# Optimization experiments

Hardware: AMD Instinct MI355X
Metric: run time of the kernel (lower is better)

Reference implementation:

```python
import jax, jax.numpy as jnp
import numpy as np

B, HORIZON, F, ORDER, K = 8192, 64, 64, 16, 256


def setup_inputs() -> dict:
    key = jax.random.key(0)
    ks = jax.random.split(key, 7)
    s = 0.05
    x = jax.random.normal(ks[0], (B, HORIZON, F), dtype=jnp.float32)
    y0 = jax.random.normal(ks[1], (B, ORDER), dtype=jnp.float32)
    kernel = jax.random.normal(ks[2], (F + ORDER, 4 * K), dtype=jnp.float32) * s
    rec_kernel = jax.random.normal(ks[3], (K, 4 * K), dtype=jnp.float32) * s
    bias = jax.random.normal(ks[4], (4 * K,), dtype=jnp.float32) * s
    dense_w = jax.random.normal(ks[5], (K, 1), dtype=jnp.float32) * s
    dense_b = jax.random.normal(ks[6], (1,), dtype=jnp.float32) * s
    return {"x": x, "y0": y0, "kernel": kernel, "rec_kernel": rec_kernel,
            "bias": bias, "dense_w": dense_w, "dense_b": dense_b}


def reference(x, y0, kernel, rec_kernel, bias, dense_w, dense_b):
    Bn = x.shape[0]
    Ku = rec_kernel.shape[0]
    h0 = jnp.zeros((Bn, Ku), x.dtype)
    c0 = jnp.zeros((Bn, Ku), x.dtype)

    def step(carry, x_t):
        h, c, yp = carry  # yp: [B, order], newest prediction first
        inp = jnp.concatenate([x_t, yp], axis=1)          # [B, F+order]
        z = inp @ kernel + h @ rec_kernel + bias          # [B, 4K]
        i, f, g, o = jnp.split(z, 4, axis=1)              # Keras gate order i,f,c,o
        i = jax.nn.sigmoid(i)
        f = jax.nn.sigmoid(f)
        g = jnp.tanh(g)
        o = jax.nn.sigmoid(o)
        c_new = f * c + i * g
        h_new = o * jnp.tanh(c_new)
        pred = h_new @ dense_w + dense_b                  # [B, 1]
        # tf.roll(shift=1)[:, 1:] then concat([pred, .]) == shift-in newest pred
        yp_new = jnp.concatenate([pred, yp[:, :-1]], axis=1)
        return (h_new, c_new, yp_new), pred

    xs = jnp.transpose(x, (1, 0, 2))                      # [horizon, B, F]
    _, preds = jax.lax.scan(step, (h0, c0, y0), xs)       # preds: [horizon, B, 1]
    return jnp.transpose(preds, (1, 0, 2))                # [B, horizon, 1]
```

## Files before the change

### kernel.cpp

```cpp
#include <hip/hip_runtime.h>
#include <stdint.h>


typedef short v8s __attribute__((ext_vector_type(8)));
typedef float v4f __attribute__((ext_vector_type(4)));

#define NKS 11
#define NKCOL 1024
#define PKR 1
#define PKL 2
#define SK0 (PKR + PKL)

__device__ __forceinline__ unsigned bf16u(float f) {
  unsigned u = __float_as_uint(f);
  return (u + 0x7FFFu + ((u >> 16) & 1u)) >> 16;
}
__device__ __forceinline__ float sigm(float x) {
  return __builtin_amdgcn_rcpf(1.f + __expf(-x));
}
__device__ __forceinline__ float tanh_(float x) {
  return 1.f - 2.f * __builtin_amdgcn_rcpf(1.f + __expf(2.f * x));
}
__device__ __forceinline__ int a_addr(int m, int k) {
  return (((m >> 4) * NKS + (k >> 5)) << 10)
       + ((((k >> 3) & 3) * 16 + (m & 15)) << 4)
       + ((k & 7) << 1);
}

__global__ void prep_w(const float* __restrict__ ker, const float* __restrict__ rec,
                       uint4* __restrict__ wsw) {
  int tid = blockIdx.x * 256 + threadIdx.x;
  int lane = tid & 63;
  int rest = tid >> 6;
  int ks = rest % NKS;
  int nt = rest / NKS;
  int n  = nt * 16 + (lane & 15);
  int k0 = ks * 32 + ((lane >> 4) & 3) * 8;
  unsigned h[8];
  #pragma unroll
  for (int j = 0; j < 8; ++j) {
    int k = k0 + j;
    float v = 0.f;
    if (k < 80)       v = ker[k * NKCOL + n];
    else if (k < 336) v = rec[(k - 80) * NKCOL + n];
    h[j] = bf16u(v);
  }
  uint4 o;
  o.x = h[0] | (h[1] << 16); o.y = h[2] | (h[3] << 16);
  o.z = h[4] | (h[5] << 16); o.w = h[6] | (h[7] << 16);
  wsw[tid] = o;
}

__global__ __launch_bounds__(512, 2)
void lstm_main(const float* __restrict__ x, const float* __restrict__ y0,
               const float* __restrict__ bias, const float* __restrict__ dw,
               const float* __restrict__ db, const v8s* __restrict__ wv,
               float* __restrict__ out) {
  __shared__ __align__(16) char a_lds[2 * NKS * 1024];
  __shared__ __align__(16) v8s w_lds[PKL * 64 * 64];
  __shared__ float predbuf[32][8];
  __shared__ float predf[32];

  const int tid  = threadIdx.x;
  const int lane = tid & 63;
  const int wave = tid >> 6;
  const int l15  = lane & 15;
  const int quad = lane >> 4;
  const int b0   = blockIdx.x * 32;

  for (int i = tid; i < 2 * NKS * 256; i += 512) ((unsigned*)a_lds)[i] = 0;
  for (int i = tid; i < PKL * 64 * 64; i += 512) {
    int ksl = i >> 12;
    int nt  = (i >> 6) & 63;
    int ln  = i & 63;
    w_lds[i] = wv[(nt * NKS + PKR + ksl) * 64 + ln];
  }

  float bias_v[8];
  int wb[8], wlo[8];
  #pragma unroll
  for (int ln = 0; ln < 8; ++ln) {
    int g = ln >> 1, s = ln & 1;
    int ntg = g * 16 + wave * 2 + s;
    wb[ln]  = ntg * NKS * 64;
    wlo[ln] = ntg * 64 + lane;
    bias_v[ln] = bias[ntg * 16 + l15];
  }
  float dw_v[2];
  dw_v[0] = dw[wave * 32 + l15];
  dw_v[1] = dw[wave * 32 + 16 + l15];
  const float dbv = db[0];

  v8s wreg[8];
  #pragma unroll
  for (int ln = 0; ln < 8; ++ln)
    wreg[ln] = wv[wb[ln] + lane];

  float cst[2][2][4];
  #pragma unroll
  for (int mt = 0; mt < 2; ++mt)
    #pragma unroll
    for (int s = 0; s < 2; ++s)
      #pragma unroll
      for (int r = 0; r < 4; ++r) cst[mt][s][r] = 0.f;

  const int ms_x  = tid >> 3;
  const int kq8_x = tid & 7;
  const int ms_y  = (tid - 256) >> 3;
  const int jj    = tid & 7;
  float4 xpa, xpb;
  if (tid < 256) {
    const float* xp = x + ((size_t)((b0 + ms_x) * 64)) * 64 + kq8_x * 8;
    xpa = ((const float4*)xp)[0];
    xpb = ((const float4*)xp)[1];
  }

  __syncthreads();

  #pragma unroll 1
  for (int t = 0; t < 64; ++t) {
    unsigned xw[4];
    unsigned short q0 = 0, q1 = 0;
    float pin = 0.f;
    if (tid < 256) {
      xw[0] = bf16u(xpa.x) | (bf16u(xpa.y) << 16);
      xw[1] = bf16u(xpa.z) | (bf16u(xpa.w) << 16);
      xw[2] = bf16u(xpb.x) | (bf16u(xpb.y) << 16);
      xw[3] = bf16u(xpb.z) | (bf16u(xpb.w) << 16);
    } else {
      if (t == 0) {
        q0 = (unsigned short)bf16u(y0[(b0 + ms_y) * 16 + 2 * jj]);
        q1 = (unsigned short)bf16u(y0[(b0 + ms_y) * 16 + 2 * jj + 1]);
      } else {
        q0 = *(const unsigned short*)(a_lds + a_addr(ms_y, 64 + 2 * jj));
        q1 = *(const unsigned short*)(a_lds + a_addr(ms_y, 64 + 2 * jj + 1));
        pin = predf[ms_y];
      }
    }
    __syncthreads();
    if (tid < 256) {
      uint4 w4; w4.x = xw[0]; w4.y = xw[1]; w4.z = xw[2]; w4.w = xw[3];
      *(uint4*)(a_lds + a_addr(ms_x, kq8_x * 8)) = w4;
    } else {
      if (t == 0) {
        *(unsigned short*)(a_lds + a_addr(ms_y, 64 + 2 * jj))     = q0;
        *(unsigned short*)(a_lds + a_addr(ms_y, 64 + 2 * jj + 1)) = q1;
      } else {
        if (jj < 7) {
          *(unsigned short*)(a_lds + a_addr(ms_y, 64 + 2 * jj + 1)) = q0;
          *(unsigned short*)(a_lds + a_addr(ms_y, 64 + 2 * jj + 2)) = q1;
        } else {
          *(unsigned short*)(a_lds + a_addr(ms_y, 79)) = q0;
        }
        if (jj == 0)
          *(unsigned short*)(a_lds + a_addr(ms_y, 64)) = (unsigned short)bf16u(pin);
      }
    }
    __syncthreads();

    if (t < 63 && tid < 256) {
      const float* xp = x + ((size_t)((b0 + ms_x) * 64 + (t + 1))) * 64 + kq8_x * 8;
      xpa = ((const float4*)xp)[0];
      xpb = ((const float4*)xp)[1];
    }

    v4f acc[2][8];
    #pragma unroll
    for (int mt = 0; mt < 2; ++mt)
      #pragma unroll
      for (int ln = 0; ln < 8; ++ln) acc[mt][ln] = v4f{0.f, 0.f, 0.f, 0.f};

    v8s bs0[8], bs1[8];
    #pragma unroll
    for (int ln = 0; ln < 8; ++ln) bs0[ln] = wv[wb[ln] + SK0 * 64 + lane];
    v8s af0 = *(const v8s*)(a_lds + (lane << 4));
    v8s af1 = *(const v8s*)(a_lds + (NKS << 10) + (lane << 4));

    #define MFMA_BLK(ksi, W8)                                                   \
      do {                                                                      \
        v8s c0 = af0, c1 = af1;                                                 \
        if ((ksi) < NKS - 1) {                                                  \
          af0 = *(const v8s*)(a_lds + (((ksi) + 1) << 10) + (lane << 4));       \
          af1 = *(const v8s*)(a_lds + ((NKS + (ksi) + 1) << 10) + (lane << 4)); \
        }                                                                       \
        _Pragma("unroll")                                                       \
        for (int ln = 0; ln < 8; ++ln) {                                        \
          acc[0][ln] = __builtin_amdgcn_mfma_f32_16x16x32_bf16(c0, W8[ln], acc[0][ln], 0, 0, 0); \
          acc[1][ln] = __builtin_amdgcn_mfma_f32_16x16x32_bf16(c1, W8[ln], acc[1][ln], 0, 0, 0); \
        }                                                                       \
      } while (0)
    #define REFILL(BUF, rks)                                                    \
      do {                                                                      \
        _Pragma("unroll")                                                       \
        for (int ln = 0; ln < 8; ++ln)                                          \
          BUF[ln] = wv[wb[ln] + (rks) * 64 + lane];                             \
      } while (0)

    MFMA_BLK(0, wreg);

    {
      v8s wl[8];
      #pragma unroll
      for (int ln = 0; ln < 8; ++ln) wl[ln] = w_lds[wlo[ln]];
      REFILL(bs1, SK0 + 1);
      MFMA_BLK(1, wl);
      #pragma unroll
      for (int ln = 0; ln < 8; ++ln) wl[ln] = w_lds[4096 + wlo[ln]];
      MFMA_BLK(2, wl);
    }

    MFMA_BLK(3, bs0);  REFILL(bs0, 5);
    MFMA_BLK(4, bs1);  REFILL(bs1, 6);
    MFMA_BLK(5, bs0);  REFILL(bs0, 7);
    MFMA_BLK(6, bs1);  REFILL(bs1, 8);
    MFMA_BLK(7, bs0);  REFILL(bs0, 9);
    MFMA_BLK(8, bs1);  REFILL(bs1, 10);
    MFMA_BLK(9, bs0);
    MFMA_BLK(10, bs1);

    #undef MFMA_BLK
    #undef REFILL

    __syncthreads();

    float padd[2][4];
    #pragma unroll
    for (int mt = 0; mt < 2; ++mt)
      #pragma unroll
      for (int r = 0; r < 4; ++r) padd[mt][r] = 0.f;

    #pragma unroll
    for (int mt = 0; mt < 2; ++mt) {
      #pragma unroll
      for (int s = 0; s < 2; ++s) {
        const int kk = 80 + wave * 32 + s * 16 + l15;
        #pragma unroll
        for (int r = 0; r < 4; ++r) {
          float zi = acc[mt][0 + s][r] + bias_v[0 + s];
          float zf = acc[mt][2 + s][r] + bias_v[2 + s];
          float zg = acc[mt][4 + s][r] + bias_v[4 + s];
          float zo = acc[mt][6 + s][r] + bias_v[6 + s];
          float is = sigm(zi), fs = sigm(zf), gs = tanh_(zg), os = sigm(zo);
          float cn = fs * cst[mt][s][r] + is * gs;
          cst[mt][s][r] = cn;
          float hh = os * tanh_(cn);
          int m = mt * 16 + quad * 4 + r;
          *(unsigned short*)(a_lds + a_addr(m, kk)) = (unsigned short)bf16u(hh);
          padd[mt][r] += hh * dw_v[s];
        }
      }
    }
    #pragma unroll
    for (int mt = 0; mt < 2; ++mt) {
      #pragma unroll
      for (int r = 0; r < 4; ++r) {
        float p = padd[mt][r];
        p += __shfl_xor(p, 1);
        p += __shfl_xor(p, 2);
        p += __shfl_xor(p, 4);
        p += __shfl_xor(p, 8);
        if (l15 == 0) predbuf[mt * 16 + quad * 4 + r][wave] = p;
      }
    }
    __syncthreads();
    if (tid < 32) {
      float p = dbv;
      #pragma unroll
      for (int w = 0; w < 8; ++w) p += predbuf[tid][w];
      out[(size_t)(b0 + tid) * 64 + t] = p;
      predf[tid] = p;
    }
    __syncthreads();
  }
}

extern "C" void kernel_launch(void* const* d_in, const int* in_sizes, int n_in,
                              void* d_out, int out_size, void* d_ws, size_t ws_size,
                              hipStream_t stream) {
  const float* x    = (const float*)d_in[0];
  const float* y0   = (const float*)d_in[1];
  const float* ker  = (const float*)d_in[2];
  const float* rec  = (const float*)d_in[3];
  const float* bias = (const float*)d_in[4];
  const float* dw   = (const float*)d_in[5];
  const float* db   = (const float*)d_in[6];

  prep_w<<<dim3(176), dim3(256), 0, stream>>>(ker, rec, (uint4*)d_ws);
  lstm_main<<<dim3(256), dim3(512), 0, stream>>>(x, y0, bias, dw, db,
                                                 (const v8s*)d_ws, (float*)d_out);
}
```

Measured before the change: 1.292 ms.

## Pin second weight k-slice in registers, prefetch across steps, and drop a barrier

```diff
diff --git a/kernel.cpp b/kernel.cpp
--- a/kernel.cpp
+++ b/kernel.cpp
@@ -7,7 +7,7 @@
 
 #define NKS 11
 #define NKCOL 1024
-#define PKR 1
+#define PKR 2
 #define PKL 2
 #define SK0 (PKR + PKL)
 
@@ -20,6 +20,12 @@
 }
 __device__ __forceinline__ float tanh_(float x) {
   return 1.f - 2.f * __builtin_amdgcn_rcpf(1.f + __expf(2.f * x));
+}
+__device__ __forceinline__ void bar_lds() {
+  __builtin_amdgcn_sched_barrier(0);
+  asm volatile("s_waitcnt lgkmcnt(0)" ::: "memory");
+  __builtin_amdgcn_s_barrier();
+  __builtin_amdgcn_sched_barrier(0);
 }
 __device__ __forceinline__ int a_addr(int m, int k) {
   return (((m >> 4) * NKS + (k >> 5)) << 10)
@@ -91,10 +97,12 @@
   dw_v[1] = dw[wave * 32 + 16 + l15];
   const float dbv = db[0];
 
-  v8s wreg[8];
-  #pragma unroll
-  for (int ln = 0; ln < 8; ++ln)
-    wreg[ln] = wv[wb[ln] + lane];
+  v8s wreg0[8], wreg1[8];
+  #pragma unroll
+  for (int ln = 0; ln < 8; ++ln) {
+    wreg0[ln] = wv[wb[ln] + lane];
+    wreg1[ln] = wv[wb[ln] + 64 + lane];
+  }
 
   float cst[2][2][4];
   #pragma unroll
@@ -103,6 +111,17 @@
     for (int s = 0; s < 2; ++s)
       #pragma unroll
       for (int r = 0; r < 4; ++r) cst[mt][s][r] = 0.f;
+
+  #define REFILL(BUF, rks)                                                    \
+    do {                                                                      \
+      _Pragma("unroll")                                                       \
+      for (int ln = 0; ln < 8; ++ln)                                          \
+        BUF[ln] = wv[wb[ln] + (rks) * 64 + lane];                             \
+    } while (0)
+
+  v8s bs0[8], bs1[8];
+  REFILL(bs0, SK0);
+  REFILL(bs1, SK0 + 1);
 
   const int ms_x  = tid >> 3;
   const int kq8_x = tid & 7;
@@ -119,33 +138,24 @@
 
   #pragma unroll 1
   for (int t = 0; t < 64; ++t) {
-    unsigned xw[4];
-    unsigned short q0 = 0, q1 = 0;
-    float pin = 0.f;
     if (tid < 256) {
-      xw[0] = bf16u(xpa.x) | (bf16u(xpa.y) << 16);
-      xw[1] = bf16u(xpa.z) | (bf16u(xpa.w) << 16);
-      xw[2] = bf16u(xpb.x) | (bf16u(xpb.y) << 16);
-      xw[3] = bf16u(xpb.z) | (bf16u(xpb.w) << 16);
-    } else {
-      if (t == 0) {
-        q0 = (unsigned short)bf16u(y0[(b0 + ms_y) * 16 + 2 * jj]);
-        q1 = (unsigned short)bf16u(y0[(b0 + ms_y) * 16 + 2 * jj + 1]);
-      } else {
-        q0 = *(const unsigned short*)(a_lds + a_addr(ms_y, 64 + 2 * jj));
-        q1 = *(const unsigned short*)(a_lds + a_addr(ms_y, 64 + 2 * jj + 1));
-        pin = predf[ms_y];
-      }
-    }
-    __syncthreads();
-    if (tid < 256) {
-      uint4 w4; w4.x = xw[0]; w4.y = xw[1]; w4.z = xw[2]; w4.w = xw[3];
+      uint4 w4;
+      w4.x = bf16u(xpa.x) | (bf16u(xpa.y) << 16);
+      w4.y = bf16u(xpa.z) | (bf16u(xpa.w) << 16);
+      w4.z = bf16u(xpb.x) | (bf16u(xpb.y) << 16);
+      w4.w = bf16u(xpb.z) | (bf16u(xpb.w) << 16);
       *(uint4*)(a_lds + a_addr(ms_x, kq8_x * 8)) = w4;
     } else {
       if (t == 0) {
+        unsigned short q0 = (unsigned short)bf16u(y0[(b0 + ms_y) * 16 + 2 * jj]);
+        unsigned short q1 = (unsigned short)bf16u(y0[(b0 + ms_y) * 16 + 2 * jj + 1]);
         *(unsigned short*)(a_lds + a_addr(ms_y, 64 + 2 * jj))     = q0;
         *(unsigned short*)(a_lds + a_addr(ms_y, 64 + 2 * jj + 1)) = q1;
       } else {
+        unsigned short q0 = *(const unsigned short*)(a_lds + a_addr(ms_y, 64 + 2 * jj));
+        unsigned short q1 = *(const unsigned short*)(a_lds + a_addr(ms_y, 64 + 2 * jj + 1));
+        float pin = predf[ms_y];
+        __builtin_amdgcn_sched_barrier(0);
         if (jj < 7) {
           *(unsigned short*)(a_lds + a_addr(ms_y, 64 + 2 * jj + 1)) = q0;
           *(unsigned short*)(a_lds + a_addr(ms_y, 64 + 2 * jj + 2)) = q1;
@@ -156,7 +166,7 @@
           *(unsigned short*)(a_lds + a_addr(ms_y, 64)) = (unsigned short)bf16u(pin);
       }
     }
-    __syncthreads();
+    bar_lds();
 
     if (t < 63 && tid < 256) {
       const float* xp = x + ((size_t)((b0 + ms_x) * 64 + (t + 1))) * 64 + kq8_x * 8;
@@ -170,9 +180,11 @@
       #pragma unroll
       for (int ln = 0; ln < 8; ++ln) acc[mt][ln] = v4f{0.f, 0.f, 0.f, 0.f};
 
-    v8s bs0[8], bs1[8];
-    #pragma unroll
-    for (int ln = 0; ln < 8; ++ln) bs0[ln] = wv[wb[ln] + SK0 * 64 + lane];
+    v8s wla[8], wlb[8];
+    #pragma unroll
+    for (int ln = 0; ln < 8; ++ln) wla[ln] = w_lds[wlo[ln]];
+    #pragma unroll
+    for (int ln = 0; ln < 8; ++ln) wlb[ln] = w_lds[4096 + wlo[ln]];
     v8s af0 = *(const v8s*)(a_lds + (lane << 4));
     v8s af1 = *(const v8s*)(a_lds + (NKS << 10) + (lane << 4));
 
@@ -189,39 +201,22 @@
           acc[1][ln] = __builtin_amdgcn_mfma_f32_16x16x32_bf16(c1, W8[ln], acc[1][ln], 0, 0, 0); \
         }                                                                       \
       } while (0)
-    #define REFILL(BUF, rks)                                                    \
-      do {                                                                      \
-        _Pragma("unroll")                                                       \
-        for (int ln = 0; ln < 8; ++ln)                                          \
-          BUF[ln] = wv[wb[ln] + (rks) * 64 + lane];                             \
-      } while (0)
-
-    MFMA_BLK(0, wreg);
-
-    {
-      v8s wl[8];
-      #pragma unroll
-      for (int ln = 0; ln < 8; ++ln) wl[ln] = w_lds[wlo[ln]];
-      REFILL(bs1, SK0 + 1);
-      MFMA_BLK(1, wl);
-      #pragma unroll
-      for (int ln = 0; ln < 8; ++ln) wl[ln] = w_lds[4096 + wlo[ln]];
-      MFMA_BLK(2, wl);
-    }
-
-    MFMA_BLK(3, bs0);  REFILL(bs0, 5);
-    MFMA_BLK(4, bs1);  REFILL(bs1, 6);
-    MFMA_BLK(5, bs0);  REFILL(bs0, 7);
-    MFMA_BLK(6, bs1);  REFILL(bs1, 8);
-    MFMA_BLK(7, bs0);  REFILL(bs0, 9);
-    MFMA_BLK(8, bs1);  REFILL(bs1, 10);
-    MFMA_BLK(9, bs0);
-    MFMA_BLK(10, bs1);
+
+    MFMA_BLK(0, wreg0);
+    MFMA_BLK(1, wreg1);
+    MFMA_BLK(2, wla);
+    MFMA_BLK(3, wlb);
+    MFMA_BLK(4, bs0);   REFILL(bs0, 6);
+    MFMA_BLK(5, bs1);   REFILL(bs1, 7);
+    MFMA_BLK(6, bs0);   REFILL(bs0, 8);
+    MFMA_BLK(7, bs1);   REFILL(bs1, 9);
+    MFMA_BLK(8, bs0);   REFILL(bs0, 10);
+    MFMA_BLK(9, bs1);   REFILL(bs1, SK0 + 1);
+    MFMA_BLK(10, bs0);  REFILL(bs0, SK0);
 
     #undef MFMA_BLK
-    #undef REFILL
-
-    __syncthreads();
+
+    bar_lds();
 
     float padd[2][4];
     #pragma unroll
@@ -262,7 +257,7 @@
         if (l15 == 0) predbuf[mt * 16 + quad * 4 + r][wave] = p;
       }
     }
-    __syncthreads();
+    bar_lds();
     if (tid < 32) {
       float p = dbv;
       #pragma unroll
@@ -270,8 +265,9 @@
       out[(size_t)(b0 + tid) * 64 + t] = p;
       predf[tid] = p;
     }
-    __syncthreads();
-  }
+    bar_lds();
+  }
+  #undef REFILL
 }
 
 extern "C" void kernel_launch(void* const* d_in, const int* in_sizes, int n_in,
```

Measured after the change: 2.136 ms. 65.4% more time.

## Split LSTM gate columns across 16 waves per block instead of 8

Applied to the files above, without the earlier changes.

```diff
diff --git a/kernel.cpp b/kernel.cpp
--- a/kernel.cpp
+++ b/kernel.cpp
@@ -7,9 +7,8 @@
 
 #define NKS 11
 #define NKCOL 1024
-#define PKR 1
 #define PKL 2
-#define SK0 (PKR + PKL)
+#define SK0 PKL
 
 __device__ __forceinline__ unsigned bf16u(float f) {
   unsigned u = __float_as_uint(f);
@@ -51,14 +50,14 @@
   wsw[tid] = o;
 }
 
-__global__ __launch_bounds__(512, 2)
+__global__ __launch_bounds__(1024, 4)
 void lstm_main(const float* __restrict__ x, const float* __restrict__ y0,
                const float* __restrict__ bias, const float* __restrict__ dw,
                const float* __restrict__ db, const v8s* __restrict__ wv,
                float* __restrict__ out) {
   __shared__ __align__(16) char a_lds[2 * NKS * 1024];
   __shared__ __align__(16) v8s w_lds[PKL * 64 * 64];
-  __shared__ float predbuf[32][8];
+  __shared__ float predbuf[32][16];
   __shared__ float predf[32];
 
   const int tid  = threadIdx.x;
@@ -68,41 +67,42 @@
   const int quad = lane >> 4;
   const int b0   = blockIdx.x * 32;
 
-  for (int i = tid; i < 2 * NKS * 256; i += 512) ((unsigned*)a_lds)[i] = 0;
-  for (int i = tid; i < PKL * 64 * 64; i += 512) {
+  for (int i = tid; i < 2 * NKS * 256; i += 1024) ((unsigned*)a_lds)[i] = 0;
+  for (int i = tid; i < PKL * 64 * 64; i += 1024) {
     int ksl = i >> 12;
     int nt  = (i >> 6) & 63;
     int ln  = i & 63;
-    w_lds[i] = wv[(nt * NKS + PKR + ksl) * 64 + ln];
-  }
-
-  float bias_v[8];
-  int wb[8], wlo[8];
+    w_lds[i] = wv[(nt * NKS + ksl) * 64 + ln];
+  }
+
+  float bias_v[4];
+  int wb[4], wlo[4];
   #pragma unroll
-  for (int ln = 0; ln < 8; ++ln) {
-    int g = ln >> 1, s = ln & 1;
-    int ntg = g * 16 + wave * 2 + s;
-    wb[ln]  = ntg * NKS * 64;
-    wlo[ln] = ntg * 64 + lane;
-    bias_v[ln] = bias[ntg * 16 + l15];
-  }
-  float dw_v[2];
-  dw_v[0] = dw[wave * 32 + l15];
-  dw_v[1] = dw[wave * 32 + 16 + l15];
-  const float dbv = db[0];
-
-  v8s wreg[8];
-  #pragma unroll
-  for (int ln = 0; ln < 8; ++ln)
-    wreg[ln] = wv[wb[ln] + lane];
-
-  float cst[2][2][4];
+  for (int g = 0; g < 4; ++g) {
+    int ntg = g * 16 + wave;
+    wb[g]  = ntg * NKS * 64;
+    wlo[g] = ntg * 64 + lane;
+    bias_v[g] = bias[ntg * 16 + l15];
+  }
+  const float dw_v = dw[wave * 16 + l15];
+  const float dbv  = db[0];
+
+  float cst[2][4];
   #pragma unroll
   for (int mt = 0; mt < 2; ++mt)
     #pragma unroll
-    for (int s = 0; s < 2; ++s)
-      #pragma unroll
-      for (int r = 0; r < 4; ++r) cst[mt][s][r] = 0.f;
+    for (int r = 0; r < 4; ++r) cst[mt][r] = 0.f;
+
+  #define REFILL(BUF, rks)                                                    \
+    do {                                                                      \
+      _Pragma("unroll")                                                       \
+      for (int g = 0; g < 4; ++g)                                             \
+        BUF[g] = wv[wb[g] + (rks) * 64 + lane];                               \
+    } while (0)
+
+  v8s bs0[4], bs1[4];
+  REFILL(bs0, SK0);
+  REFILL(bs1, SK0 + 1);
 
   const int ms_x  = tid >> 3;
   const int kq8_x = tid & 7;
@@ -127,7 +127,7 @@
       xw[1] = bf16u(xpa.z) | (bf16u(xpa.w) << 16);
       xw[2] = bf16u(xpb.x) | (bf16u(xpb.y) << 16);
       xw[3] = bf16u(xpb.z) | (bf16u(xpb.w) << 16);
-    } else {
+    } else if (tid < 512) {
       if (t == 0) {
         q0 = (unsigned short)bf16u(y0[(b0 + ms_y) * 16 + 2 * jj]);
         q1 = (unsigned short)bf16u(y0[(b0 + ms_y) * 16 + 2 * jj + 1]);
@@ -141,7 +141,7 @@
     if (tid < 256) {
       uint4 w4; w4.x = xw[0]; w4.y = xw[1]; w4.z = xw[2]; w4.w = xw[3];
       *(uint4*)(a_lds + a_addr(ms_x, kq8_x * 8)) = w4;
-    } else {
+    } else if (tid < 512) {
       if (t == 0) {
         *(unsigned short*)(a_lds + a_addr(ms_y, 64 + 2 * jj))     = q0;
         *(unsigned short*)(a_lds + a_addr(ms_y, 64 + 2 * jj + 1)) = q1;
@@ -158,25 +158,16 @@
     }
     __syncthreads();
 
-    if (t < 63 && tid < 256) {
-      const float* xp = x + ((size_t)((b0 + ms_x) * 64 + (t + 1))) * 64 + kq8_x * 8;
-      xpa = ((const float4*)xp)[0];
-      xpb = ((const float4*)xp)[1];
-    }
-
-    v4f acc[2][8];
+    v4f acc[2][4];
     #pragma unroll
     for (int mt = 0; mt < 2; ++mt)
       #pragma unroll
-      for (int ln = 0; ln < 8; ++ln) acc[mt][ln] = v4f{0.f, 0.f, 0.f, 0.f};
-
-    v8s bs0[8], bs1[8];
-    #pragma unroll
-    for (int ln = 0; ln < 8; ++ln) bs0[ln] = wv[wb[ln] + SK0 * 64 + lane];
+      for (int g = 0; g < 4; ++g) acc[mt][g] = v4f{0.f, 0.f, 0.f, 0.f};
+
     v8s af0 = *(const v8s*)(a_lds + (lane << 4));
     v8s af1 = *(const v8s*)(a_lds + (NKS << 10) + (lane << 4));
 
-    #define MFMA_BLK(ksi, W8)                                                   \
+    #define MFMA_BLK(ksi, W4)                                                   \
       do {                                                                      \
         v8s c0 = af0, c1 = af1;                                                 \
         if ((ksi) < NKS - 1) {                                                  \
@@ -184,70 +175,59 @@
           af1 = *(const v8s*)(a_lds + ((NKS + (ksi) + 1) << 10) + (lane << 4)); \
         }                                                                       \
         _Pragma("unroll")                                                       \
-        for (int ln = 0; ln < 8; ++ln) {                                        \
-          acc[0][ln] = __builtin_amdgcn_mfma_f32_16x16x32_bf16(c0, W8[ln], acc[0][ln], 0, 0, 0); \
-          acc[1][ln] = __builtin_amdgcn_mfma_f32_16x16x32_bf16(c1, W8[ln], acc[1][ln], 0, 0, 0); \
+        for (int g = 0; g < 4; ++g) {                                           \
+          acc[0][g] = __builtin_amdgcn_mfma_f32_16x16x32_bf16(c0, W4[g], acc[0][g], 0, 0, 0); \
+          acc[1][g] = __builtin_amdgcn_mfma_f32_16x16x32_bf16(c1, W4[g], acc[1][g], 0, 0, 0); \
         }                                                                       \
       } while (0)
-    #define REFILL(BUF, rks)                                                    \
-      do {                                                                      \
-        _Pragma("unroll")                                                       \
-        for (int ln = 0; ln < 8; ++ln)                                          \
-          BUF[ln] = wv[wb[ln] + (rks) * 64 + lane];                             \
-      } while (0)
-
-    MFMA_BLK(0, wreg);
 
     {
-      v8s wl[8];
-      #pragma unroll
-      for (int ln = 0; ln < 8; ++ln) wl[ln] = w_lds[wlo[ln]];
-      REFILL(bs1, SK0 + 1);
-      MFMA_BLK(1, wl);
-      #pragma unroll
-      for (int ln = 0; ln < 8; ++ln) wl[ln] = w_lds[4096 + wlo[ln]];
-      MFMA_BLK(2, wl);
-    }
-
-    MFMA_BLK(3, bs0);  REFILL(bs0, 5);
-    MFMA_BLK(4, bs1);  REFILL(bs1, 6);
-    MFMA_BLK(5, bs0);  REFILL(bs0, 7);
-    MFMA_BLK(6, bs1);  REFILL(bs1, 8);
-    MFMA_BLK(7, bs0);  REFILL(bs0, 9);
-    MFMA_BLK(8, bs1);  REFILL(bs1, 10);
-    MFMA_BLK(9, bs0);
-    MFMA_BLK(10, bs1);
+      v8s wl0[4];
+      #pragma unroll
+      for (int g = 0; g < 4; ++g) wl0[g] = w_lds[wlo[g]];
+      MFMA_BLK(0, wl0);
+      v8s wl1[4];
+      #pragma unroll
+      for (int g = 0; g < 4; ++g) wl1[g] = w_lds[4096 + wlo[g]];
+      MFMA_BLK(1, wl1);
+    }
+    MFMA_BLK(2, bs0);   REFILL(bs0, 4);
+    MFMA_BLK(3, bs1);   REFILL(bs1, 5);
+    MFMA_BLK(4, bs0);   REFILL(bs0, 6);
+    MFMA_BLK(5, bs1);   REFILL(bs1, 7);
+    MFMA_BLK(6, bs0);   REFILL(bs0, 8);
+    MFMA_BLK(7, bs1);   REFILL(bs1, 9);
+    MFMA_BLK(8, bs0);   REFILL(bs0, 10);
+    MFMA_BLK(9, bs1);   REFILL(bs1, SK0 + 1);
+    MFMA_BLK(10, bs0);  REFILL(bs0, SK0);
 
     #undef MFMA_BLK
-    #undef REFILL
-
-    __syncthreads();
-
+
+    __syncthreads();
+
+    if (t < 63 && tid < 256) {
+      const float* xp = x + ((size_t)((b0 + ms_x) * 64 + (t + 1))) * 64 + kq8_x * 8;
+      xpa = ((const float4*)xp)[0];
+      xpb = ((const float4*)xp)[1];
+    }
+
+    const int kk = 80 + wave * 16 + l15;
     float padd[2][4];
     #pragma unroll
-    for (int mt = 0; mt < 2; ++mt)
-      #pragma unroll
-      for (int r = 0; r < 4; ++r) padd[mt][r] = 0.f;
-
-    #pragma unroll
     for (int mt = 0; mt < 2; ++mt) {
       #pragma unroll
-      for (int s = 0; s < 2; ++s) {
-        const int kk = 80 + wave * 32 + s * 16 + l15;
-        #pragma unroll
-        for (int r = 0; r < 4; ++r) {
-          float zi = acc[mt][0 + s][r] + bias_v[0 + s];
-          float zf = acc[mt][2 + s][r] + bias_v[2 + s];
-          float zg = acc[mt][4 + s][r] + bias_v[4 + s];
-          float zo = acc[mt][6 + s][r] + bias_v[6 + s];
-          float is = sigm(zi), fs = sigm(zf), gs = tanh_(zg), os = sigm(zo);
-          float cn = fs * cst[mt][s][r] + is * gs;
-          cst[mt][s][r] = cn;
-          float hh = os * tanh_(cn);
-          int m = mt * 16 + quad * 4 + r;
-          *(unsigned short*)(a_lds + a_addr(m, kk)) = (unsigned short)bf16u(hh);
-          padd[mt][r] += hh * dw_v[s];
-        }
+      for (int r = 0; r < 4; ++r) {
+        float zi = acc[mt][0][r] + bias_v[0];
+        float zf = acc[mt][1][r] + bias_v[1];
+        float zg = acc[mt][2][r] + bias_v[2];
+        float zo = acc[mt][3][r] + bias_v[3];
+        float is = sigm(zi), fs = sigm(zf), gs = tanh_(zg), os = sigm(zo);
+        float cn = fs * cst[mt][r] + is * gs;
+        cst[mt][r] = cn;
+        float hh = os * tanh_(cn);
+        int m = mt * 16 + quad * 4 + r;
+        *(unsigned short*)(a_lds + a_addr(m, kk)) = (unsigned short)bf16u(hh);
+        padd[mt][r] = hh * dw_v;
       }
     }
     #pragma unroll
@@ -266,12 +246,13 @@
     if (tid < 32) {
       float p = dbv;
       #pragma unroll
-      for (int w = 0; w < 8; ++w) p += predbuf[tid][w];
+      for (int w = 0; w < 16; ++w) p += predbuf[tid][w];
       out[(size_t)(b0 + tid) * 64 + t] = p;
       predf[tid] = p;
     }
     __syncthreads();
   }
+  #undef REFILL
 }
 
 extern "C" void kernel_launch(void* const* d_in, const int* in_sizes, int n_in,
@@ -286,6 +267,6 @@
   const float* db   = (const float*)d_in[6];
 
   prep_w<<<dim3(176), dim3(256), 0, stream>>>(ker, rec, (uint4*)d_ws);
-  lstm_main<<<dim3(256), dim3(512), 0, stream>>>(x, y0, bias, dw, db,
-                                                 (const v8s*)d_ws, (float*)d_out);
-}
+  lstm_main<<<dim3(256), dim3(1024), 0, stream>>>(x, y0, bias, dw, db,
+                                                  (const v8s*)d_ws, (float*)d_out);
+}
```

Result: slower. 1.578 ms (+22.1%).

## Double batch rows per block to reuse streamed weights across four M-tiles

Applied to the files above, without the earlier changes.

```diff
diff --git a/kernel.cpp b/kernel.cpp
--- a/kernel.cpp
+++ b/kernel.cpp
@@ -7,9 +7,7 @@
 
 #define NKS 11
 #define NKCOL 1024
-#define PKR 1
-#define PKL 2
-#define SK0 (PKR + PKL)
+#define MT 4
 
 __device__ __forceinline__ unsigned bf16u(float f) {
   unsigned u = __float_as_uint(f);
@@ -56,24 +54,22 @@
                const float* __restrict__ bias, const float* __restrict__ dw,
                const float* __restrict__ db, const v8s* __restrict__ wv,
                float* __restrict__ out) {
-  __shared__ __align__(16) char a_lds[2 * NKS * 1024];
-  __shared__ __align__(16) v8s w_lds[PKL * 64 * 64];
-  __shared__ float predbuf[32][8];
-  __shared__ float predf[32];
+  __shared__ __align__(16) char a_lds[MT * NKS * 1024];
+  __shared__ __align__(16) v8s w_lds[64 * 64];
+  __shared__ float predbuf[64][8];
+  __shared__ float predf[64];
 
   const int tid  = threadIdx.x;
   const int lane = tid & 63;
   const int wave = tid >> 6;
   const int l15  = lane & 15;
   const int quad = lane >> 4;
-  const int b0   = blockIdx.x * 32;
-
-  for (int i = tid; i < 2 * NKS * 256; i += 512) ((unsigned*)a_lds)[i] = 0;
-  for (int i = tid; i < PKL * 64 * 64; i += 512) {
-    int ksl = i >> 12;
-    int nt  = (i >> 6) & 63;
-    int ln  = i & 63;
-    w_lds[i] = wv[(nt * NKS + PKR + ksl) * 64 + ln];
+  const int b0   = blockIdx.x * 64;
+
+  for (int i = tid; i < MT * NKS * 256; i += 512) ((unsigned*)a_lds)[i] = 0;
+  for (int i = tid; i < 64 * 64; i += 512) {
+    int nt = i >> 6, ln = i & 63;
+    w_lds[i] = wv[(nt * NKS) * 64 + ln];
   }
 
   float bias_v[8];
@@ -91,26 +87,30 @@
   dw_v[1] = dw[wave * 32 + 16 + l15];
   const float dbv = db[0];
 
-  v8s wreg[8];
+  float cst[MT][2][4];
   #pragma unroll
-  for (int ln = 0; ln < 8; ++ln)
-    wreg[ln] = wv[wb[ln] + lane];
-
-  float cst[2][2][4];
-  #pragma unroll
-  for (int mt = 0; mt < 2; ++mt)
+  for (int mt = 0; mt < MT; ++mt)
     #pragma unroll
     for (int s = 0; s < 2; ++s)
       #pragma unroll
       for (int r = 0; r < 4; ++r) cst[mt][s][r] = 0.f;
 
-  const int ms_x  = tid >> 3;
-  const int kq8_x = tid & 7;
-  const int ms_y  = (tid - 256) >> 3;
-  const int jj    = tid & 7;
+  #define REFILL(BUF, rks)                                                    \
+    do {                                                                      \
+      _Pragma("unroll")                                                       \
+      for (int ln = 0; ln < 8; ++ln)                                          \
+        BUF[ln] = wv[wb[ln] + (rks) * 64 + lane];                             \
+    } while (0)
+
+  v8s bs0[8], bs1[8];
+  REFILL(bs0, 1);
+  REFILL(bs1, 2);
+
+  const int ms  = tid >> 3;
+  const int kq8 = tid & 7;
   float4 xpa, xpb;
-  if (tid < 256) {
-    const float* xp = x + ((size_t)((b0 + ms_x) * 64)) * 64 + kq8_x * 8;
+  {
+    const float* xp = x + ((size_t)((b0 + ms) * 64)) * 64 + kq8 * 8;
     xpa = ((const float4*)xp)[0];
     xpb = ((const float4*)xp)[1];
   }
@@ -120,117 +120,103 @@
   #pragma unroll 1
   for (int t = 0; t < 64; ++t) {
     unsigned xw[4];
-    unsigned short q0 = 0, q1 = 0;
+    xw[0] = bf16u(xpa.x) | (bf16u(xpa.y) << 16);
+    xw[1] = bf16u(xpa.z) | (bf16u(xpa.w) << 16);
+    xw[2] = bf16u(xpb.x) | (bf16u(xpb.y) << 16);
+    xw[3] = bf16u(xpb.z) | (bf16u(xpb.w) << 16);
+    unsigned short q0, q1;
     float pin = 0.f;
-    if (tid < 256) {
-      xw[0] = bf16u(xpa.x) | (bf16u(xpa.y) << 16);
-      xw[1] = bf16u(xpa.z) | (bf16u(xpa.w) << 16);
-      xw[2] = bf16u(xpb.x) | (bf16u(xpb.y) << 16);
-      xw[3] = bf16u(xpb.z) | (bf16u(xpb.w) << 16);
+    if (t == 0) {
+      q0 = (unsigned short)bf16u(y0[(b0 + ms) * 16 + 2 * kq8]);
+      q1 = (unsigned short)bf16u(y0[(b0 + ms) * 16 + 2 * kq8 + 1]);
     } else {
-      if (t == 0) {
-        q0 = (unsigned short)bf16u(y0[(b0 + ms_y) * 16 + 2 * jj]);
-        q1 = (unsigned short)bf16u(y0[(b0 + ms_y) * 16 + 2 * jj + 1]);
+      q0 = *(const unsigned short*)(a_lds + a_addr(ms, 64 + 2 * kq8));
+      q1 = *(const unsigned short*)(a_lds + a_addr(ms, 64 + 2 * kq8 + 1));
+      pin = predf[ms];
+    }
+    __syncthreads();
+    {
+      uint4 w4; w4.x = xw[0]; w4.y = xw[1]; w4.z = xw[2]; w4.w = xw[3];
+      *(uint4*)(a_lds + a_addr(ms, kq8 * 8)) = w4;
+    }
+    if (t == 0) {
+      *(unsigned short*)(a_lds + a_addr(ms, 64 + 2 * kq8))     = q0;
+      *(unsigned short*)(a_lds + a_addr(ms, 64 + 2 * kq8 + 1)) = q1;
+    } else {
+      if (kq8 < 7) {
+        *(unsigned short*)(a_lds + a_addr(ms, 64 + 2 * kq8 + 1)) = q0;
+        *(unsigned short*)(a_lds + a_addr(ms, 64 + 2 * kq8 + 2)) = q1;
       } else {
-        q0 = *(const unsigned short*)(a_lds + a_addr(ms_y, 64 + 2 * jj));
-        q1 = *(const unsigned short*)(a_lds + a_addr(ms_y, 64 + 2 * jj + 1));
-        pin = predf[ms_y];
+        *(unsigned short*)(a_lds + a_addr(ms, 79)) = q0;
       }
-    }
-    __syncthreads();
-    if (tid < 256) {
-      uint4 w4; w4.x = xw[0]; w4.y = xw[1]; w4.z = xw[2]; w4.w = xw[3];
-      *(uint4*)(a_lds + a_addr(ms_x, kq8_x * 8)) = w4;
-    } else {
-      if (t == 0) {
-        *(unsigned short*)(a_lds + a_addr(ms_y, 64 + 2 * jj))     = q0;
-        *(unsigned short*)(a_lds + a_addr(ms_y, 64 + 2 * jj + 1)) = q1;
-      } else {
-        if (jj < 7) {
-          *(unsigned short*)(a_lds + a_addr(ms_y, 64 + 2 * jj + 1)) = q0;
-          *(unsigned short*)(a_lds + a_addr(ms_y, 64 + 2 * jj + 2)) = q1;
-        } else {
-          *(unsigned short*)(a_lds + a_addr(ms_y, 79)) = q0;
-        }
-        if (jj == 0)
-          *(unsigned short*)(a_lds + a_addr(ms_y, 64)) = (unsigned short)bf16u(pin);
-      }
-    }
-    __syncthreads();
-
-    if (t < 63 && tid < 256) {
-      const float* xp = x + ((size_t)((b0 + ms_x) * 64 + (t + 1))) * 64 + kq8_x * 8;
-      xpa = ((const float4*)xp)[0];
-      xpb = ((const float4*)xp)[1];
-    }
-
-    v4f acc[2][8];
-    #pragma unroll
-    for (int mt = 0; mt < 2; ++mt)
+      if (kq8 == 0)
+        *(unsigned short*)(a_lds + a_addr(ms, 64)) = (unsigned short)bf16u(pin);
+    }
+    __syncthreads();
+
+    v4f acc[MT][8];
+    #pragma unroll
+    for (int mt = 0; mt < MT; ++mt)
       #pragma unroll
       for (int ln = 0; ln < 8; ++ln) acc[mt][ln] = v4f{0.f, 0.f, 0.f, 0.f};
 
-    v8s bs0[8], bs1[8];
-    #pragma unroll
-    for (int ln = 0; ln < 8; ++ln) bs0[ln] = wv[wb[ln] + SK0 * 64 + lane];
-    v8s af0 = *(const v8s*)(a_lds + (lane << 4));
-    v8s af1 = *(const v8s*)(a_lds + (NKS << 10) + (lane << 4));
+    v8s af[MT];
+    #pragma unroll
+    for (int mt = 0; mt < MT; ++mt)
+      af[mt] = *(const v8s*)(a_lds + ((mt * NKS) << 10) + (lane << 4));
 
     #define MFMA_BLK(ksi, W8)                                                   \
       do {                                                                      \
-        v8s c0 = af0, c1 = af1;                                                 \
+        v8s c0 = af[0], c1 = af[1], c2 = af[2], c3 = af[3];                     \
         if ((ksi) < NKS - 1) {                                                  \
-          af0 = *(const v8s*)(a_lds + (((ksi) + 1) << 10) + (lane << 4));       \
-          af1 = *(const v8s*)(a_lds + ((NKS + (ksi) + 1) << 10) + (lane << 4)); \
+          _Pragma("unroll")                                                     \
+          for (int mt = 0; mt < MT; ++mt)                                       \
+            af[mt] = *(const v8s*)(a_lds + ((mt * NKS + (ksi) + 1) << 10) + (lane << 4)); \
         }                                                                       \
         _Pragma("unroll")                                                       \
         for (int ln = 0; ln < 8; ++ln) {                                        \
           acc[0][ln] = __builtin_amdgcn_mfma_f32_16x16x32_bf16(c0, W8[ln], acc[0][ln], 0, 0, 0); \
           acc[1][ln] = __builtin_amdgcn_mfma_f32_16x16x32_bf16(c1, W8[ln], acc[1][ln], 0, 0, 0); \
+          acc[2][ln] = __builtin_amdgcn_mfma_f32_16x16x32_bf16(c2, W8[ln], acc[2][ln], 0, 0, 0); \
+          acc[3][ln] = __builtin_amdgcn_mfma_f32_16x16x32_bf16(c3, W8[ln], acc[3][ln], 0, 0, 0); \
         }                                                                       \
       } while (0)
-    #define REFILL(BUF, rks)                                                    \
-      do {                                                                      \
-        _Pragma("unroll")                                                       \
-        for (int ln = 0; ln < 8; ++ln)                                          \
-          BUF[ln] = wv[wb[ln] + (rks) * 64 + lane];                             \
-      } while (0)
-
-    MFMA_BLK(0, wreg);
 
     {
       v8s wl[8];
       #pragma unroll
       for (int ln = 0; ln < 8; ++ln) wl[ln] = w_lds[wlo[ln]];
-      REFILL(bs1, SK0 + 1);
-      MFMA_BLK(1, wl);
-      #pragma unroll
-      for (int ln = 0; ln < 8; ++ln) wl[ln] = w_lds[4096 + wlo[ln]];
-      MFMA_BLK(2, wl);
-    }
-
-    MFMA_BLK(3, bs0);  REFILL(bs0, 5);
-    MFMA_BLK(4, bs1);  REFILL(bs1, 6);
-    MFMA_BLK(5, bs0);  REFILL(bs0, 7);
-    MFMA_BLK(6, bs1);  REFILL(bs1, 8);
-    MFMA_BLK(7, bs0);  REFILL(bs0, 9);
-    MFMA_BLK(8, bs1);  REFILL(bs1, 10);
-    MFMA_BLK(9, bs0);
-    MFMA_BLK(10, bs1);
+      MFMA_BLK(0, wl);
+    }
+    MFMA_BLK(1, bs0);   REFILL(bs0, 3);
+    MFMA_BLK(2, bs1);   REFILL(bs1, 4);
+    MFMA_BLK(3, bs0);   REFILL(bs0, 5);
+    MFMA_BLK(4, bs1);   REFILL(bs1, 6);
+    MFMA_BLK(5, bs0);   REFILL(bs0, 7);
+    MFMA_BLK(6, bs1);   REFILL(bs1, 8);
+    MFMA_BLK(7, bs0);   REFILL(bs0, 9);
+    MFMA_BLK(8, bs1);   REFILL(bs1, 10);
+    MFMA_BLK(9, bs0);   REFILL(bs0, 1);
+    MFMA_BLK(10, bs1);  REFILL(bs1, 2);
 
     #undef MFMA_BLK
-    #undef REFILL
-
-    __syncthreads();
-
-    float padd[2][4];
-    #pragma unroll
-    for (int mt = 0; mt < 2; ++mt)
+
+    __syncthreads();
+
+    if (t < 63) {
+      const float* xp = x + ((size_t)((b0 + ms) * 64 + (t + 1))) * 64 + kq8 * 8;
+      xpa = ((const float4*)xp)[0];
+      xpb = ((const float4*)xp)[1];
+    }
+
+    float padd[MT][4];
+    #pragma unroll
+    for (int mt = 0; mt < MT; ++mt)
       #pragma unroll
       for (int r = 0; r < 4; ++r) padd[mt][r] = 0.f;
 
     #pragma unroll
-    for (int mt = 0; mt < 2; ++mt) {
+    for (int mt = 0; mt < MT; ++mt) {
       #pragma unroll
       for (int s = 0; s < 2; ++s) {
         const int kk = 80 + wave * 32 + s * 16 + l15;
@@ -251,7 +237,7 @@
       }
     }
     #pragma unroll
-    for (int mt = 0; mt < 2; ++mt) {
+    for (int mt = 0; mt < MT; ++mt) {
       #pragma unroll
       for (int r = 0; r < 4; ++r) {
         float p = padd[mt][r];
@@ -263,7 +249,7 @@
       }
     }
     __syncthreads();
-    if (tid < 32) {
+    if (tid < 64) {
       float p = dbv;
       #pragma unroll
       for (int w = 0; w < 8; ++w) p += predbuf[tid][w];
@@ -272,6 +258,7 @@
     }
     __syncthreads();
   }
+  #undef REFILL
 }
 
 extern "C" void kernel_launch(void* const* d_in, const int* in_sizes, int n_in,
@@ -286,6 +273,6 @@
   const float* db   = (const float*)d_in[6];
 
   prep_w<<<dim3(176), dim3(256), 0, stream>>>(ker, rec, (uint4*)d_ws);
-  lstm_main<<<dim3(256), dim3(512), 0, stream>>>(x, y0, bias, dw, db,
+  lstm_main<<<dim3(128), dim3(512), 0, stream>>>(x, y0, bias, dw, db,
                                                  (const v8s*)d_ws, (float*)d_out);
 }
```

Result: slower. 2.212 ms (+71.3%).
